# Performance work log

Measured on AMD Instinct MI355X. Metric: run time of the kernel, lower is better.

## Reference

```python
import jax, jax.numpy as jnp
import numpy as np

RADIUS = 1.0
SIGMA = 0.16                 # w = relu(1 - d^2 / sigma), as in EPN's linear interpolation
N_NEIGHBOR = 32
KERNEL_CONDENSE_RATIO = 0.7


def ball_query(xyz, radius, n_neighbor):
    # xyz: [b,3,p]; stride==1 so query set == support set.
    pts = xyz.transpose(0, 2, 1)                      # [b,p,3]
    sq = jnp.sum(pts * pts, -1)                       # [b,p]
    d2 = sq[:, :, None] + sq[:, None, :] - 2.0 * jnp.einsum('bqd,bpd->bqp', pts, pts)
    p = pts.shape[1]
    # first n_neighbor points (in index order) within the ball; pad with first valid
    keys = jnp.where(d2 < radius * radius, jnp.arange(p)[None, None, :], p)   # [b,q,p] int
    vals, _ = jax.lax.top_k(-keys, n_neighbor)        # n_neighbor smallest keys
    cand = -vals                                      # candidate indices, ascending
    idx = jnp.where(cand < p, cand, cand[..., :1])    # self (d2=0) is always valid
    grouped = jax.vmap(lambda pt, i: pt[i])(pts, idx)  # [b,q,nn,3]
    rel = grouped - pts[:, :, None, :]                # local (relative) coordinates
    return idx, rel.transpose(0, 3, 1, 2)             # idx [b,q,nn], rel [b,3,q,nn]


def forward(xyz, feats, W, anchors, kernels):
    b, c_in, p, na = feats.shape
    ks = kernels.shape[0]
    idx, gxyz = ball_query(xyz, RADIUS, N_NEIGHBOR)   # [b,p,nn], [b,3,p,nn]
    # anchor-rotated kernel points: [na,ks,3]
    rk = jnp.einsum('aij,kj->aki', anchors, kernels)
    # squared distances neighbor <-> rotated kernel point, via |x|^2+|k|^2-2<x,k>
    dot = jnp.einsum('aki,bipn->bakpn', rk, gxyz)     # [b,na,ks,p,nn]
    d2 = (jnp.sum(gxyz * gxyz, 1)[:, None, None]
          + jnp.sum(rk * rk, -1)[None, :, :, None, None]
          - 2.0 * dot)
    inter_w = jax.nn.relu(1.0 - d2 / SIGMA)           # [b,na,ks,p,nn]
    # gather neighbor features: [b,c,p,nn,na]
    gf = jax.vmap(lambda f, i: f[:, i, :])(feats, idx)
    # kernel-weighted neighbor aggregation -> [b,c,ks,p,na]
    new_feats = jnp.einsum('bcpna,bakpn->bckpa', gf, inter_w)
    # BasicSO3Conv: W [dim_out, c_in*ks] @ [b, c_in*ks, p*na]
    dim_out = W.shape[0]
    out = jnp.einsum('oc,bcm->bom', W, new_feats.reshape(b, c_in * ks, p * na))
    return out.reshape(b, dim_out, p, na)


def setup_inputs() -> dict:
    key = jax.random.key(0)
    k1, k2, k3, k4, k5, k6 = jax.random.split(key, 6)
    b, p, c_in, c_out, na, ks = 1, 1024, 32, 64, 60, 24
    xyz = jax.random.normal(k1, (b, 3, p), dtype=jnp.float32)
    feats = jax.random.normal(k2, (b, c_in, p, na), dtype=jnp.float32)
    W = jax.random.normal(k3, (c_out, c_in * ks), dtype=jnp.float32) / np.float32(np.sqrt(c_in * ks))
    # proper rotation matrices (stand-in for the icosahedral anchors)
    A = jax.random.normal(k4, (na, 3, 3), dtype=jnp.float32)
    Q, _ = jnp.linalg.qr(A)
    anchors = Q * jnp.sign(jnp.linalg.det(Q))[:, None, None]
    # kernel points uniform in ball of radius 0.7*RADIUS (stand-in for the ply kernel)
    dirs = jax.random.normal(k5, (ks, 3), dtype=jnp.float32)
    dirs = dirs / jnp.linalg.norm(dirs, axis=-1, keepdims=True)
    r = (jax.random.uniform(k6, (ks, 1), dtype=jnp.float32) ** (1.0 / 3.0)) * (KERNEL_CONDENSE_RATIO * RADIUS)
    kernels = dirs * r
    return {"xyz": xyz, "feats": feats, "W": W, "anchors": anchors, "kernels": kernels}


def reference(xyz, feats, W, anchors, kernels):
    return forward(xyz, feats, W, anchors, kernels)
```

## Files before the change

kernel.cpp:

```cpp
#include <hip/hip_runtime.h>

typedef __attribute__((ext_vector_type(8))) short short8;
typedef __attribute__((ext_vector_type(4))) float f32x4;
typedef __attribute__((ext_vector_type(4))) unsigned int uint4v;

#define P_PTS   1024
#define NN      32
#define NA      60
#define KS      24
#define CIN     32
#define COUT    64
#define AC      12
#define NCH     5
#define SA      968
#define GF_SHORTS (AC*16*72)

union frag_u { uint4v u; short8 s; };

__device__ __forceinline__ unsigned short f2bf(float f) {
  unsigned int u = __float_as_uint(f);
  u += 0x7FFFu + ((u >> 16) & 1u);
  return (unsigned short)(u >> 16);
}
__device__ __forceinline__ unsigned int bfpair(float a, float b) {
  unsigned int ua = __float_as_uint(a) + 0x8000u;
  unsigned int ub = __float_as_uint(b) + 0x8000u;
  return __builtin_amdgcn_perm(ub, ua, 0x07060302u);
}
__device__ __forceinline__ void ilv(unsigned int u, unsigned int v,
                                    unsigned int& lo, unsigned int& hi) {
  lo = __builtin_amdgcn_perm(v, u, 0x05040100u);
  hi = __builtin_amdgcn_perm(v, u, 0x07060302u);
}

__device__ __forceinline__ float wcalc(const float4 rk, const float4 rl) {
  return fmaxf(0.0f, fmaf(rk.x, rl.x, fmaf(rk.y, rl.y, fmaf(rk.z, rl.z, rk.w + rl.w))));
}

#define SETUP_BLOCKS 1310

__global__ __launch_bounds__(256) void setup_kernel(
    const float* __restrict__ xyz, const float* __restrict__ feats,
    const float* __restrict__ Wm, const float* __restrict__ anchors,
    const float* __restrict__ kernels, int* __restrict__ ws_idx,
    unsigned short* __restrict__ ws_ft, unsigned short* __restrict__ ws_wbf,
    float4* __restrict__ ws_rk4)
{
  const int b   = blockIdx.x;
  const int tid = threadIdx.x;

  __shared__ float sx[P_PTS], sy[P_PTS], sz[P_PTS], sq[P_PTS];
  __shared__ int s_loc[4][NN];
  __shared__ unsigned short s_t[CIN*NA];

  if (b < 256) {
    for (int i = tid; i < P_PTS; i += 256) {
      float x = xyz[i], y = xyz[P_PTS + i], z = xyz[2*P_PTS + i];
      sx[i] = x; sy[i] = y; sz[i] = z;
      sq[i] = x*x + y*y + z*z;
    }
    __syncthreads();
    const int wave = tid >> 6, lane = tid & 63;
    const int q = b*4 + wave;
    const float xq = sx[q], yq = sy[q], zq = sz[q], sqq = sq[q];
    int cnt = 0;
    for (int jb = 0; jb < P_PTS; jb += 64) {
      const int j = jb + lane;
      const float d2 = sqq + sq[j] - 2.0f*(xq*sx[j] + yq*sy[j] + zq*sz[j]);
      const bool pred = d2 < 1.0f;
      const unsigned long long mask = __ballot(pred);
      if (pred) {
        const int slot = cnt + __popcll(mask & ((1ull << lane) - 1ull));
        if (slot < NN) s_loc[wave][slot] = j;
      }
      cnt += (int)__popcll(mask);
      if (cnt >= NN) break;
    }
    __syncthreads();
    const int cntc = cnt < NN ? cnt : NN;
    if (lane >= cntc && lane < NN) s_loc[wave][lane] = s_loc[wave][0];
    __syncthreads();
    if (lane < NN) ws_idx[q*NN + lane] = s_loc[wave][lane];
  } else if (b < 1280) {
    const int p = b - 256;
    for (int e = tid; e < CIN*NA; e += 256) {
      const int c = e / NA, a = e - c*NA;
      s_t[e] = f2bf(feats[c*(P_PTS*NA) + p*NA + a]);
    }
    __syncthreads();
    unsigned int* out32 = (unsigned int*)(ws_ft + p*(CIN*NA));
    for (int e = tid; e < (CIN*NA)/2; e += 256) {
      const int a = e >> 4, cu = e & 15;
      const unsigned int lo = s_t[(2*cu    )*NA + a];
      const unsigned int hi = s_t[(2*cu + 1)*NA + a];
      out32[a*16 + cu] = lo | (hi << 16);
    }
  } else if (b < 1304) {
    const int t = (b - 1280)*256 + tid;
    const int w = t / 1536;
    const int r = t - w*1536;
    const int s = r >> 6;
    const int lane = r & 63;
    const int quad = lane >> 4, lq = lane & 15;
    const int o = w*16 + lq;
    unsigned short h[8];
    #pragma unroll
    for (int j = 0; j < 8; ++j)
      h[j] = f2bf(Wm[o*(CIN*KS) + (quad*8 + j)*KS + s]);
    *(uint4*)(ws_wbf + (size_t)t*8) = *(const uint4*)h;
  } else {
    const int u = (b - 1304)*256 + tid;
    if (u < NA*KS) {
      const int a = u / KS, k = u - a*KS;
      const float rx = anchors[a*9+0]*kernels[k*3+0] + anchors[a*9+1]*kernels[k*3+1] + anchors[a*9+2]*kernels[k*3+2];
      const float ry = anchors[a*9+3]*kernels[k*3+0] + anchors[a*9+4]*kernels[k*3+1] + anchors[a*9+5]*kernels[k*3+2];
      const float rz = anchors[a*9+6]*kernels[k*3+0] + anchors[a*9+7]*kernels[k*3+1] + anchors[a*9+8]*kernels[k*3+2];
      ws_rk4[u] = make_float4(12.5f*rx, 12.5f*ry, 12.5f*rz,
                              1.0f - 6.25f*(rx*rx + ry*ry + rz*rz));
    }
  }
}

__global__ __launch_bounds__(256, 4) void conv_mfma(
    const float* __restrict__ xyz, const unsigned short* __restrict__ ft,
    const unsigned short* __restrict__ Wf, const int* __restrict__ g_idx,
    const float4* __restrict__ g_rk4, float* __restrict__ out)
{
  const int p    = blockIdx.x;
  const int a0   = blockIdx.y * AC;
  const int tid  = threadIdx.x;
  const int wave = tid >> 6;
  const int lane = tid & 63;
  const int quad = lane >> 4;
  const int lq   = lane & 15;

  __shared__ __align__(16) unsigned short s_buf[GF_SHORTS];
  __shared__ __align__(16) float4 s_rel4[NN];
  __shared__ __align__(16) float4 s_rk4[AC*KS];
  __shared__ int s_idx[NN];

  if (tid < NN) {
    const int j = g_idx[p*NN + tid];
    s_idx[tid] = j;
    const float rx = xyz[j]           - xyz[p];
    const float ry = xyz[P_PTS + j]   - xyz[P_PTS + p];
    const float rz = xyz[2*P_PTS + j] - xyz[2*P_PTS + p];
    s_rel4[tid] = make_float4(rx, ry, rz, -6.25f*(rx*rx + ry*ry + rz*rz));
  }
  for (int e = tid; e < AC*KS; e += 256) s_rk4[e] = g_rk4[a0*KS + e];
  __syncthreads();

  const int np = (tid >> 2) & 15;
  const int ce = tid & 3;
  const int i0 = s_idx[2*np];
  const int i1 = s_idx[2*np + 1];
  const unsigned short* ft0 = ft + (size_t)i0*(CIN*NA) + a0*CIN + ce*8;
  const unsigned short* ft1 = ft + (size_t)i1*(CIN*NA) + a0*CIN + ce*8;
  #pragma unroll
  for (int i = 0; i < 3; ++i) {
    const int a = i*4 + wave;
    const uint4 u = *(const uint4*)(ft0 + a*CIN);
    const uint4 v = *(const uint4*)(ft1 + a*CIN);
    unsigned short* dst = &s_buf[a*1152 + np*72 + ce*16];
    uint4v w0, w1;
    unsigned int d0, d1;
    ilv(u.x, v.x, d0, d1); w0[0] = d0; w0[1] = d1;
    ilv(u.y, v.y, d0, d1); w0[2] = d0; w0[3] = d1;
    ilv(u.z, v.z, d0, d1); w1[0] = d0; w1[1] = d1;
    ilv(u.w, v.w, d0, d1); w1[2] = d0; w1[3] = d1;
    *(uint4v*)(dst)     = w0;
    *(uint4v*)(dst + 8) = w1;
  }
  __syncthreads();

  const unsigned int* bufd = (const unsigned int*)s_buf;
  f32x4 acc1[3][2][2] = {};
  #pragma unroll
  for (int t = 0; t < 3; ++t) {
    const int a = wave*3 + t;
    const int based = a*576 + quad*144 + lq;
    frag_u af0, af1;
    #pragma unroll
    for (int i = 0; i < 4; ++i) {
      af0.u[i] = bufd[based + 36*i];
      af1.u[i] = bufd[based + 36*i + 16];
    }
    const int k1 = (lq < 8) ? (16 + lq) : 23;
    const float4 rk0 = s_rk4[a*KS + lq];
    const float4 rk1 = s_rk4[a*KS + k1];
    frag_u b0, b1;
    #pragma unroll
    for (int i = 0; i < 4; ++i) {
      const float4 rA = s_rel4[quad*8 + 2*i];
      const float4 rB = s_rel4[quad*8 + 2*i + 1];
      b0.u[i] = bfpair(wcalc(rk0, rA), wcalc(rk0, rB));
      b1.u[i] = bfpair(wcalc(rk1, rA), wcalc(rk1, rB));
    }
    acc1[t][0][0] = __builtin_amdgcn_mfma_f32_16x16x32_bf16(af0.s, b0.s, acc1[t][0][0], 0, 0, 0);
    acc1[t][0][1] = __builtin_amdgcn_mfma_f32_16x16x32_bf16(af0.s, b1.s, acc1[t][0][1], 0, 0, 0);
    acc1[t][1][0] = __builtin_amdgcn_mfma_f32_16x16x32_bf16(af1.s, b0.s, acc1[t][1][0], 0, 0, 0);
    acc1[t][1][1] = __builtin_amdgcn_mfma_f32_16x16x32_bf16(af1.s, b1.s, acc1[t][1][1], 0, 0, 0);
  }
  __syncthreads();

  #pragma unroll
  for (int t = 0; t < 3; ++t) {
    const int a = wave*3 + t;
    unsigned short* row = &s_buf[a*SA];
    uint2 pk;
    pk.x = bfpair(acc1[t][0][0][0], acc1[t][0][0][1]);
    pk.y = bfpair(acc1[t][0][0][2], acc1[t][0][0][3]);
    *(uint2*)&row[lq*40 + quad*4] = pk;
    pk.x = bfpair(acc1[t][1][0][0], acc1[t][1][0][1]);
    pk.y = bfpair(acc1[t][1][0][2], acc1[t][1][0][3]);
    *(uint2*)&row[lq*40 + 16 + quad*4] = pk;
    if (lq < 8) {
      pk.x = bfpair(acc1[t][0][1][0], acc1[t][0][1][1]);
      pk.y = bfpair(acc1[t][0][1][2], acc1[t][0][1][3]);
      *(uint2*)&row[(16+lq)*40 + quad*4] = pk;
      pk.x = bfpair(acc1[t][1][1][0], acc1[t][1][1][1]);
      pk.y = bfpair(acc1[t][1][1][2], acc1[t][1][1][3]);
      *(uint2*)&row[(16+lq)*40 + 16 + quad*4] = pk;
    }
  }
  __syncthreads();

  const int acl = (lq < AC) ? lq : (AC - 1);
  const unsigned short* wptr = Wf + (size_t)wave*(24*512) + lane*8;
  const unsigned short* nptr = &s_buf[acl*SA + quad*8];
  f32x4 accA = {0.f,0.f,0.f,0.f}, accB = {0.f,0.f,0.f,0.f};
  #pragma unroll 4
  for (int s = 0; s < 24; s += 2) {
    const short8 aw0 = *(const short8*)(wptr + s*512);
    const short8 bn0 = *(const short8*)(nptr + s*40);
    const short8 aw1 = *(const short8*)(wptr + s*512 + 512);
    const short8 bn1 = *(const short8*)(nptr + s*40 + 40);
    accA = __builtin_amdgcn_mfma_f32_16x16x32_bf16(aw0, bn0, accA, 0, 0, 0);
    accB = __builtin_amdgcn_mfma_f32_16x16x32_bf16(aw1, bn1, accB, 0, 0, 0);
  }

  if (lq < AC) {
    const int ob = wave*16 + quad*4;
    #pragma unroll
    for (int r = 0; r < 4; ++r)
      out[(size_t)(ob + r)*(P_PTS*NA) + p*NA + a0 + lq] = accA[r] + accB[r];
  }
}

extern "C" void kernel_launch(void* const* d_in, const int* in_sizes, int n_in,
                              void* d_out, int out_size, void* d_ws, size_t ws_size,
                              hipStream_t stream) {
  const float* xyz     = (const float*)d_in[0];
  const float* feats   = (const float*)d_in[1];
  const float* Wm      = (const float*)d_in[2];
  const float* anchors = (const float*)d_in[3];
  const float* kernels = (const float*)d_in[4];
  float* out = (float*)d_out;

  unsigned short* ws_wbf = (unsigned short*)d_ws;
  int*    ws_idx = (int*)((char*)d_ws + 98304);
  float4* ws_rk4 = (float4*)((char*)d_ws + 98304 + 131072);
  unsigned short* ws_ft = (unsigned short*)((char*)d_ws + 98304 + 131072 + 23040);

  hipLaunchKernelGGL(setup_kernel, dim3(SETUP_BLOCKS), dim3(256), 0, stream,
                     xyz, feats, Wm, anchors, kernels, ws_idx, ws_ft, ws_wbf, ws_rk4);
  hipLaunchKernelGGL(conv_mfma, dim3(P_PTS, NCH), dim3(256), 0, stream,
                     xyz, ws_ft, ws_wbf, ws_idx, ws_rk4, out);
}
```

Before: 109.4 us.

## Loop over anchor chunks inside each block and prefetch next chunk's gathered features

The grid drops from (P, NCH) to P blocks, and each block now loops over all five anchor chunks. This reuses the neighbor indices, relative coordinates and W pointers across chunks. The next chunk's gathered feature loads are issued into registers before the second-stage MFMA loop, so global latency overlaps with compute. The cost is 5x fewer blocks (1024 on the device), less parallelism and extra barriers per chunk.

```diff
diff --git a/kernel.cpp b/kernel.cpp
--- a/kernel.cpp
+++ b/kernel.cpp
@@ -127,7 +127,6 @@
     const float4* __restrict__ g_rk4, float* __restrict__ out)
 {
   const int p    = blockIdx.x;
-  const int a0   = blockIdx.y * AC;
   const int tid  = threadIdx.x;
   const int wave = tid >> 6;
   const int lane = tid & 63;
@@ -137,113 +136,131 @@
   __shared__ __align__(16) unsigned short s_buf[GF_SHORTS];
   __shared__ __align__(16) float4 s_rel4[NN];
   __shared__ __align__(16) float4 s_rk4[AC*KS];
-  __shared__ int s_idx[NN];
 
   if (tid < NN) {
     const int j = g_idx[p*NN + tid];
-    s_idx[tid] = j;
     const float rx = xyz[j]           - xyz[p];
     const float ry = xyz[P_PTS + j]   - xyz[P_PTS + p];
     const float rz = xyz[2*P_PTS + j] - xyz[2*P_PTS + p];
     s_rel4[tid] = make_float4(rx, ry, rz, -6.25f*(rx*rx + ry*ry + rz*rz));
   }
-  for (int e = tid; e < AC*KS; e += 256) s_rk4[e] = g_rk4[a0*KS + e];
-  __syncthreads();
-
   const int np = (tid >> 2) & 15;
   const int ce = tid & 3;
-  const int i0 = s_idx[2*np];
-  const int i1 = s_idx[2*np + 1];
-  const unsigned short* ft0 = ft + (size_t)i0*(CIN*NA) + a0*CIN + ce*8;
-  const unsigned short* ft1 = ft + (size_t)i1*(CIN*NA) + a0*CIN + ce*8;
+  const int i0 = g_idx[p*NN + 2*np];
+  const int i1 = g_idx[p*NN + 2*np + 1];
+  const unsigned short* ft0 = ft + (size_t)i0*(CIN*NA) + ce*8;
+  const unsigned short* ft1 = ft + (size_t)i1*(CIN*NA) + ce*8;
+
+  uint4 pu[3], pv[3];
   #pragma unroll
   for (int i = 0; i < 3; ++i) {
-    const int a = i*4 + wave;
-    const uint4 u = *(const uint4*)(ft0 + a*CIN);
-    const uint4 v = *(const uint4*)(ft1 + a*CIN);
-    unsigned short* dst = &s_buf[a*1152 + np*72 + ce*16];
-    uint4v w0, w1;
-    unsigned int d0, d1;
-    ilv(u.x, v.x, d0, d1); w0[0] = d0; w0[1] = d1;
-    ilv(u.y, v.y, d0, d1); w0[2] = d0; w0[3] = d1;
-    ilv(u.z, v.z, d0, d1); w1[0] = d0; w1[1] = d1;
-    ilv(u.w, v.w, d0, d1); w1[2] = d0; w1[3] = d1;
-    *(uint4v*)(dst)     = w0;
-    *(uint4v*)(dst + 8) = w1;
-  }
-  __syncthreads();
+    const int ag = i*4 + wave;
+    pu[i] = *(const uint4*)(ft0 + ag*CIN);
+    pv[i] = *(const uint4*)(ft1 + ag*CIN);
+  }
 
   const unsigned int* bufd = (const unsigned int*)s_buf;
-  f32x4 acc1[3][2][2] = {};
-  #pragma unroll
-  for (int t = 0; t < 3; ++t) {
-    const int a = wave*3 + t;
-    const int based = a*576 + quad*144 + lq;
-    frag_u af0, af1;
-    #pragma unroll
-    for (int i = 0; i < 4; ++i) {
-      af0.u[i] = bufd[based + 36*i];
-      af1.u[i] = bufd[based + 36*i + 16];
-    }
-    const int k1 = (lq < 8) ? (16 + lq) : 23;
-    const float4 rk0 = s_rk4[a*KS + lq];
-    const float4 rk1 = s_rk4[a*KS + k1];
-    frag_u b0, b1;
-    #pragma unroll
-    for (int i = 0; i < 4; ++i) {
-      const float4 rA = s_rel4[quad*8 + 2*i];
-      const float4 rB = s_rel4[quad*8 + 2*i + 1];
-      b0.u[i] = bfpair(wcalc(rk0, rA), wcalc(rk0, rB));
-      b1.u[i] = bfpair(wcalc(rk1, rA), wcalc(rk1, rB));
-    }
-    acc1[t][0][0] = __builtin_amdgcn_mfma_f32_16x16x32_bf16(af0.s, b0.s, acc1[t][0][0], 0, 0, 0);
-    acc1[t][0][1] = __builtin_amdgcn_mfma_f32_16x16x32_bf16(af0.s, b1.s, acc1[t][0][1], 0, 0, 0);
-    acc1[t][1][0] = __builtin_amdgcn_mfma_f32_16x16x32_bf16(af1.s, b0.s, acc1[t][1][0], 0, 0, 0);
-    acc1[t][1][1] = __builtin_amdgcn_mfma_f32_16x16x32_bf16(af1.s, b1.s, acc1[t][1][1], 0, 0, 0);
-  }
-  __syncthreads();
-
-  #pragma unroll
-  for (int t = 0; t < 3; ++t) {
-    const int a = wave*3 + t;
-    unsigned short* row = &s_buf[a*SA];
-    uint2 pk;
-    pk.x = bfpair(acc1[t][0][0][0], acc1[t][0][0][1]);
-    pk.y = bfpair(acc1[t][0][0][2], acc1[t][0][0][3]);
-    *(uint2*)&row[lq*40 + quad*4] = pk;
-    pk.x = bfpair(acc1[t][1][0][0], acc1[t][1][0][1]);
-    pk.y = bfpair(acc1[t][1][0][2], acc1[t][1][0][3]);
-    *(uint2*)&row[lq*40 + 16 + quad*4] = pk;
-    if (lq < 8) {
-      pk.x = bfpair(acc1[t][0][1][0], acc1[t][0][1][1]);
-      pk.y = bfpair(acc1[t][0][1][2], acc1[t][0][1][3]);
-      *(uint2*)&row[(16+lq)*40 + quad*4] = pk;
-      pk.x = bfpair(acc1[t][1][1][0], acc1[t][1][1][1]);
-      pk.y = bfpair(acc1[t][1][1][2], acc1[t][1][1][3]);
-      *(uint2*)&row[(16+lq)*40 + 16 + quad*4] = pk;
-    }
-  }
-  __syncthreads();
-
-  const int acl = (lq < AC) ? lq : (AC - 1);
   const unsigned short* wptr = Wf + (size_t)wave*(24*512) + lane*8;
-  const unsigned short* nptr = &s_buf[acl*SA + quad*8];
-  f32x4 accA = {0.f,0.f,0.f,0.f}, accB = {0.f,0.f,0.f,0.f};
-  #pragma unroll 4
-  for (int s = 0; s < 24; s += 2) {
-    const short8 aw0 = *(const short8*)(wptr + s*512);
-    const short8 bn0 = *(const short8*)(nptr + s*40);
-    const short8 aw1 = *(const short8*)(wptr + s*512 + 512);
-    const short8 bn1 = *(const short8*)(nptr + s*40 + 40);
-    accA = __builtin_amdgcn_mfma_f32_16x16x32_bf16(aw0, bn0, accA, 0, 0, 0);
-    accB = __builtin_amdgcn_mfma_f32_16x16x32_bf16(aw1, bn1, accB, 0, 0, 0);
-  }
-
-  if (lq < AC) {
-    const int ob = wave*16 + quad*4;
-    #pragma unroll
-    for (int r = 0; r < 4; ++r)
-      out[(size_t)(ob + r)*(P_PTS*NA) + p*NA + a0 + lq] = accA[r] + accB[r];
+
+  for (int ch = 0; ch < NCH; ++ch) {
+    const int a0 = ch * AC;
+
+    for (int e = tid; e < AC*KS; e += 256) s_rk4[e] = g_rk4[a0*KS + e];
+    #pragma unroll
+    for (int i = 0; i < 3; ++i) {
+      const int a = i*4 + wave;
+      unsigned short* dst = &s_buf[a*1152 + np*72 + ce*16];
+      uint4v w0, w1;
+      unsigned int d0, d1;
+      ilv(pu[i].x, pv[i].x, d0, d1); w0[0] = d0; w0[1] = d1;
+      ilv(pu[i].y, pv[i].y, d0, d1); w0[2] = d0; w0[3] = d1;
+      ilv(pu[i].z, pv[i].z, d0, d1); w1[0] = d0; w1[1] = d1;
+      ilv(pu[i].w, pv[i].w, d0, d1); w1[2] = d0; w1[3] = d1;
+      *(uint4v*)(dst)     = w0;
+      *(uint4v*)(dst + 8) = w1;
+    }
+    __syncthreads();
+
+    f32x4 acc1[3][2][2] = {};
+    #pragma unroll
+    for (int t = 0; t < 3; ++t) {
+      const int a = wave*3 + t;
+      const int based = a*576 + quad*144 + lq;
+      frag_u af0, af1;
+      #pragma unroll
+      for (int i = 0; i < 4; ++i) {
+        af0.u[i] = bufd[based + 36*i];
+        af1.u[i] = bufd[based + 36*i + 16];
+      }
+      const int k1 = (lq < 8) ? (16 + lq) : 23;
+      const float4 rk0 = s_rk4[a*KS + lq];
+      const float4 rk1 = s_rk4[a*KS + k1];
+      frag_u b0, b1;
+      #pragma unroll
+      for (int i = 0; i < 4; ++i) {
+        const float4 rA = s_rel4[quad*8 + 2*i];
+        const float4 rB = s_rel4[quad*8 + 2*i + 1];
+        b0.u[i] = bfpair(wcalc(rk0, rA), wcalc(rk0, rB));
+        b1.u[i] = bfpair(wcalc(rk1, rA), wcalc(rk1, rB));
+      }
+      acc1[t][0][0] = __builtin_amdgcn_mfma_f32_16x16x32_bf16(af0.s, b0.s, acc1[t][0][0], 0, 0, 0);
+      acc1[t][0][1] = __builtin_amdgcn_mfma_f32_16x16x32_bf16(af0.s, b1.s, acc1[t][0][1], 0, 0, 0);
+      acc1[t][1][0] = __builtin_amdgcn_mfma_f32_16x16x32_bf16(af1.s, b0.s, acc1[t][1][0], 0, 0, 0);
+      acc1[t][1][1] = __builtin_amdgcn_mfma_f32_16x16x32_bf16(af1.s, b1.s, acc1[t][1][1], 0, 0, 0);
+    }
+    __syncthreads();
+
+    #pragma unroll
+    for (int t = 0; t < 3; ++t) {
+      const int a = wave*3 + t;
+      unsigned short* row = &s_buf[a*SA];
+      uint2 pk;
+      pk.x = bfpair(acc1[t][0][0][0], acc1[t][0][0][1]);
+      pk.y = bfpair(acc1[t][0][0][2], acc1[t][0][0][3]);
+      *(uint2*)&row[lq*40 + quad*4] = pk;
+      pk.x = bfpair(acc1[t][1][0][0], acc1[t][1][0][1]);
+      pk.y = bfpair(acc1[t][1][0][2], acc1[t][1][0][3]);
+      *(uint2*)&row[lq*40 + 16 + quad*4] = pk;
+      if (lq < 8) {
+        pk.x = bfpair(acc1[t][0][1][0], acc1[t][0][1][1]);
+        pk.y = bfpair(acc1[t][0][1][2], acc1[t][0][1][3]);
+        *(uint2*)&row[(16+lq)*40 + quad*4] = pk;
+        pk.x = bfpair(acc1[t][1][1][0], acc1[t][1][1][1]);
+        pk.y = bfpair(acc1[t][1][1][2], acc1[t][1][1][3]);
+        *(uint2*)&row[(16+lq)*40 + 16 + quad*4] = pk;
+      }
+    }
+    __syncthreads();
+
+    if (ch + 1 < NCH) {
+      #pragma unroll
+      for (int i = 0; i < 3; ++i) {
+        const int ag = (ch + 1)*AC + i*4 + wave;
+        pu[i] = *(const uint4*)(ft0 + ag*CIN);
+        pv[i] = *(const uint4*)(ft1 + ag*CIN);
+      }
+    }
+
+    const int acl = (lq < AC) ? lq : (AC - 1);
+    const unsigned short* nptr = &s_buf[acl*SA + quad*8];
+    f32x4 accA = {0.f,0.f,0.f,0.f}, accB = {0.f,0.f,0.f,0.f};
+    #pragma unroll 4
+    for (int s = 0; s < 24; s += 2) {
+      const short8 aw0 = *(const short8*)(wptr + s*512);
+      const short8 bn0 = *(const short8*)(nptr + s*40);
+      const short8 aw1 = *(const short8*)(wptr + s*512 + 512);
+      const short8 bn1 = *(const short8*)(nptr + s*40 + 40);
+      accA = __builtin_amdgcn_mfma_f32_16x16x32_bf16(aw0, bn0, accA, 0, 0, 0);
+      accB = __builtin_amdgcn_mfma_f32_16x16x32_bf16(aw1, bn1, accB, 0, 0, 0);
+    }
+
+    if (lq < AC) {
+      const int ob = wave*16 + quad*4;
+      #pragma unroll
+      for (int r = 0; r < 4; ++r)
+        out[(size_t)(ob + r)*(P_PTS*NA) + p*NA + a0 + lq] = accA[r] + accB[r];
+    }
+    __syncthreads();
   }
 }
 
@@ -264,6 +281,6 @@
 
   hipLaunchKernelGGL(setup_kernel, dim3(SETUP_BLOCKS), dim3(256), 0, stream,
                      xyz, feats, Wm, anchors, kernels, ws_idx, ws_ft, ws_wbf, ws_rk4);
-  hipLaunchKernelGGL(conv_mfma, dim3(P_PTS, NCH), dim3(256), 0, stream,
+  hipLaunchKernelGGL(conv_mfma, dim3(P_PTS), dim3(256), 0, stream,
                      xyz, ws_ft, ws_wbf, ws_idx, ws_rk4, out);
 }
```

After: 111.6 us. 1.02x slower.
